# Kernel tuning notes

Hardware: AMD Instinct MI355X
Metric: run time of the kernel (lower is better)

## Reference

```python
import jax, jax.numpy as jnp
import numpy as np

NEG = -1e9


def _siglu(x):
    return x * jax.nn.sigmoid(x)


def setup_inputs() -> dict:
    key = jax.random.key(0)
    ks = jax.random.split(key, 10)
    B, S, M, D = 2, 2048, 64, 1024
    sc = 0.02
    return {
        "tokens": jax.random.normal(ks[0], (B, S, D), jnp.float32),
        "memory": jax.random.normal(ks[1], (B, M, D), jnp.float32),
        "Wq": jax.random.normal(ks[2], (D, D), jnp.float32) * sc,
        "bq": jnp.zeros((D,), jnp.float32),
        "Wk": jax.random.normal(ks[3], (D, D), jnp.float32) * sc,
        "bk": jnp.zeros((D,), jnp.float32),
        "Wv": jax.random.normal(ks[4], (D, D), jnp.float32) * sc,
        "bv": jnp.zeros((D,), jnp.float32),
        "Wo": jax.random.normal(ks[5], (D, D), jnp.float32) * sc,
        "bo": jnp.zeros((D,), jnp.float32),
        "pool_q": jax.random.normal(ks[6], (M, D), jnp.float32),
        "cell_W": jax.random.normal(ks[7], (2 * D, 2 * D), jnp.float32) * sc,
        "cell_b": jnp.zeros((2 * D,), jnp.float32),
    }


def reference(tokens, memory, Wq, bq, Wk, bk, Wv, bv, Wo, bo, pool_q, cell_W, cell_b):
    B, S, D = tokens.shape
    M = memory.shape[1]
    H = 16
    hd = D // H
    T = M + S

    x = jnp.concatenate([memory, tokens], axis=1)  # (B, T, D)

    # combined causal mask: memory rows/cols fully visible, token block causal
    tok_mask = jnp.triu(jnp.full((S, S), NEG, jnp.float32), k=1)
    mask = jnp.zeros((T, T), jnp.float32).at[M:, M:].set(tok_mask)  # (T, T)

    def heads(w, b):
        return (x @ w.T + b).reshape(B, T, H, hd).transpose(0, 2, 1, 3)

    q = heads(Wq, bq)  # (B, H, T, hd)
    k = heads(Wk, bk)
    v = heads(Wv, bv)

    scores = jnp.einsum("bhqd,bhkd->bhqk", q, k) * (hd ** -0.5) + mask
    attn = jax.nn.softmax(scores, axis=-1)
    ctx = jnp.einsum("bhqk,bhkd->bhqd", attn, v)
    ctx = ctx.transpose(0, 2, 1, 3).reshape(B, T, D)
    attn_out = ctx @ Wo.T + bo

    x = x + attn_out  # residual
    mem_out = x[:, :M]  # (B, M, D)
    tok_out = x[:, M:]  # (B, S, D)

    # attention pooling: one learnable query per memory slot
    pscores = jnp.einsum("md,bsd->bms", pool_q, tok_out) * (D ** -0.5)
    pweights = jax.nn.softmax(pscores, axis=-1)
    summary = jnp.einsum("bms,bsd->bmd", pweights, tok_out)  # (B, M, D)

    # MinimalRNNCell (siglu-gated) applied per memory slot
    combined = jnp.concatenate([mem_out, summary], axis=-1)  # (B, M, 2D)
    update = combined @ cell_W.T + cell_b
    gate, cand = jnp.split(update, 2, axis=-1)
    gate = jax.nn.sigmoid(gate)
    new_memory = mem_out * gate + (1.0 - gate) * _siglu(cand)

    return tok_out, new_memory
```

## Files before the change

kernel.cpp:

```cpp
#include <hip/hip_runtime.h>
#include <hip/hip_bf16.h>

#define B_  2
#define S_  2048
#define M_  64
#define D_  1024
#define T_  2112
#define H_  16
#define HD_ 64
#define BT_ (B_*T_)
#define NEGBIG (-1e9f)
#define LOG2E 1.44269504f

typedef float f32x4  __attribute__((ext_vector_type(4)));
typedef short short8 __attribute__((ext_vector_type(8)));
typedef unsigned short u16x4 __attribute__((ext_vector_type(4)));
typedef __bf16 bf16x8 __attribute__((ext_vector_type(8)));

typedef unsigned short TileBuf[2][128][64];

static __device__ __forceinline__ unsigned short bf16_of(float f) {
  __hip_bfloat16 h = __float2bfloat16(f);
  return __builtin_bit_cast(unsigned short, h);
}

static __device__ __forceinline__ f32x4 mfma_bf16(short8 a, short8 b, f32x4 c) {
  return __builtin_amdgcn_mfma_f32_16x16x32_bf16(
      __builtin_bit_cast(bf16x8, a), __builtin_bit_cast(bf16x8, b), c, 0, 0, 0);
}

static __device__ __forceinline__ void gload16(const void* g, void* lds) {
  __builtin_amdgcn_global_load_lds(
      (const __attribute__((address_space(1))) unsigned int*)g,
      (__attribute__((address_space(3))) unsigned int*)lds, 16, 0, 0);
}


__global__ void k_build_x(const float* __restrict__ tokens,
                          const float* __restrict__ memory,
                          unsigned short* __restrict__ xb) {
  for (int i = blockIdx.x * blockDim.x + threadIdx.x; i < BT_ * D_;
       i += gridDim.x * blockDim.x) {
    int b = i / (T_ * D_);
    int rem = i - b * (T_ * D_);
    int t = rem / D_;
    int d = rem - t * D_;
    float v = (t < M_) ? memory[((size_t)b * M_ + t) * D_ + d]
                       : tokens[((size_t)b * S_ + (t - M_)) * D_ + d];
    xb[i] = bf16_of(v);
  }
}

__global__ void k_cast_all(const float* __restrict__ Wq, const float* __restrict__ Wk,
                           const float* __restrict__ Wv, const float* __restrict__ Wo,
                           const float* __restrict__ cW, const float* __restrict__ pq,
                           unsigned short* __restrict__ Wqkvb, unsigned short* __restrict__ Wob,
                           unsigned short* __restrict__ cWb, unsigned short* __restrict__ pqb) {
  const int NW = D_ * D_;
  const int NC = 4 * D_ * D_;
  const int NP = M_ * D_;
  const int total = 4 * NW + NC + NP;
  for (int i = blockIdx.x * blockDim.x + threadIdx.x; i < total;
       i += gridDim.x * blockDim.x) {
    if (i < 3 * NW) {
      int which = i >> 20, j = i & (NW - 1);
      const float* s = (which == 0) ? Wq : (which == 1) ? Wk : Wv;
      Wqkvb[i] = bf16_of(s[j]);
    } else if (i < 4 * NW) {
      int j = i - 3 * NW;
      Wob[j] = bf16_of(Wo[j]);
    } else if (i < 4 * NW + NC) {
      int j = i - 4 * NW;
      cWb[j] = bf16_of(cW[j]);
    } else {
      int j = i - 4 * NW - NC;
      pqb[j] = bf16_of(pq[j] * 0.03125f * LOG2E);
    }
  }
}

__device__ __forceinline__ void gemm128_core(TileBuf& As, TileBuf& Bs,
                                             const unsigned short* __restrict__ A,
                                             const unsigned short* __restrict__ BT,
                                             int K, int m0, int n0,
                                             f32x4 acc[4][4]) {
  const int tid = threadIdx.x;
  const int w = tid >> 6, l = tid & 63;
  const int wr = w >> 1, wc = w & 1;
  const int lr = l & 15, lg = l >> 4;
  f32x4 z; z[0] = z[1] = z[2] = z[3] = 0.f;
#pragma unroll
  for (int i = 0; i < 4; i++)
#pragma unroll
    for (int j = 0; j < 4; j++) acc[i][j] = z;

  auto stage = [&](int buf, int k0) {
#pragma unroll
    for (int c = 0; c < 4; c++) {
      int rbase = c * 32 + w * 8;
      int rr = rbase + (l >> 3);
      int u = (l & 7) ^ (rr & 7);
      gload16(&A[(size_t)(m0 + rr) * K + k0 + u * 8], &As[buf][rbase][0]);
      gload16(&BT[(size_t)(n0 + rr) * K + k0 + u * 8], &Bs[buf][rbase][0]);
    }
  };

  stage(0, 0);
  int cur = 0;
  const int NK = K >> 6;
  for (int kt = 0; kt < NK; kt++) {
    if (kt + 1 < NK) {
      stage(cur ^ 1, (kt + 1) << 6);
      asm volatile("s_waitcnt vmcnt(8)" ::: "memory");
    } else {
      asm volatile("s_waitcnt vmcnt(0)" ::: "memory");
    }
    __builtin_amdgcn_s_barrier();

    short8 a[4][2], b[4][2];
#pragma unroll
    for (int i = 0; i < 4; i++) {
      int row = wr * 64 + i * 16 + lr;
      int sw = row & 7;
#pragma unroll
      for (int kk = 0; kk < 2; kk++)
        a[i][kk] = *(const short8*)&As[cur][row][(((kk << 2) | lg) ^ sw) * 8];
    }
#pragma unroll
    for (int j = 0; j < 4; j++) {
      int row = wc * 64 + j * 16 + lr;
      int sw = row & 7;
#pragma unroll
      for (int kk = 0; kk < 2; kk++)
        b[j][kk] = *(const short8*)&Bs[cur][row][(((kk << 2) | lg) ^ sw) * 8];
    }
    __builtin_amdgcn_s_setprio(1);
#pragma unroll
    for (int kk = 0; kk < 2; kk++)
#pragma unroll
      for (int i = 0; i < 4; i++)
#pragma unroll
        for (int j = 0; j < 4; j++)
          acc[i][j] = mfma_bf16(a[i][kk], b[j][kk], acc[i][j]);
    __builtin_amdgcn_s_setprio(0);

    __builtin_amdgcn_s_barrier();
    cur ^= 1;
  }
}

__device__ __forceinline__ void gemm_core(const unsigned short* __restrict__ A,
                                          const unsigned short* __restrict__ BT,
                                          int ldk, int Klen, int m0, int n0,
                                          f32x4 acc[4]) {
  __shared__ __align__(16) unsigned short As[64][40];
  __shared__ __align__(16) unsigned short Bs[64][40];
  const int tid = threadIdx.x;
  const int w = tid >> 6, l = tid & 63;
  const int sr = tid >> 2, sc = (tid & 3) * 8;
  f32x4 z; z[0] = z[1] = z[2] = z[3] = 0.f;
  acc[0] = acc[1] = acc[2] = acc[3] = z;
  for (int k0 = 0; k0 < Klen; k0 += 32) {
    __syncthreads();
    *(short8*)&As[sr][sc] = *(const short8*)&A[(size_t)(m0 + sr) * ldk + k0 + sc];
    *(short8*)&Bs[sr][sc] = *(const short8*)&BT[(size_t)(n0 + sr) * ldk + k0 + sc];
    __syncthreads();
    short8 a = *(const short8*)&As[w * 16 + (l & 15)][(l >> 4) * 8];
#pragma unroll
    for (int n = 0; n < 4; n++) {
      short8 b = *(const short8*)&Bs[n * 16 + (l & 15)][(l >> 4) * 8];
      acc[n] = mfma_bf16(a, b, acc[n]);
    }
  }
}

__global__ __launch_bounds__(256) void k_qk(
    const unsigned short* __restrict__ xb, const unsigned short* __restrict__ Wqkvb,
    const float* __restrict__ bq, const float* __restrict__ bk,
    unsigned short* __restrict__ qg, unsigned short* __restrict__ kg) {
  __shared__ __align__(16) TileBuf As;
  __shared__ __align__(16) TileBuf Bs;
  const int which = blockIdx.x >> 3;
  const unsigned short* W = Wqkvb + (size_t)which * D_ * D_;
  const float* bias = (which == 0) ? bq : bk;
  f32x4 acc[4][4];
  const int m0 = blockIdx.y * 128, n0 = (blockIdx.x & 7) * 128;
  gemm128_core(As, Bs, xb, W, D_, m0, n0, acc);
  const int tid = threadIdx.x, w = tid >> 6, l = tid & 63;
  const int wr = w >> 1, wc = w & 1;
#pragma unroll
  for (int i = 0; i < 4; i++) {
#pragma unroll
    for (int j = 0; j < 4; j++) {
#pragma unroll
      for (int r = 0; r < 4; r++) {
        int m = m0 + wr * 64 + i * 16 + (l >> 4) * 4 + r;
        int c = n0 + wc * 64 + j * 16 + (l & 15);
        int b = (m >= T_) ? 1 : 0;
        int t = m - b * T_;
        int h = c >> 6, dh = c & 63;
        int bh = b * H_ + h;
        float v = acc[i][j][r] + bias[c];
        if (which == 0)
          qg[((size_t)bh * T_ + t) * HD_ + dh] = bf16_of(v * 0.125f * LOG2E);
        else
          kg[((size_t)bh * T_ + t) * HD_ + dh] = bf16_of(v);
      }
    }
  }
}

__global__ __launch_bounds__(256) void k_v(
    const unsigned short* __restrict__ xb, const unsigned short* __restrict__ Wqkvb,
    const float* __restrict__ bv, unsigned short* __restrict__ vTg) {
  __shared__ __align__(16) TileBuf As;
  __shared__ __align__(16) TileBuf Bs;
  f32x4 acc[4][4];
  const int m0 = blockIdx.y * 128, n0 = blockIdx.x * 128;
  gemm128_core(As, Bs, xb, Wqkvb + (size_t)2 * D_ * D_, D_, m0, n0, acc);
  const int tid = threadIdx.x, w = tid >> 6, l = tid & 63;
  const int wr = w >> 1, wc = w & 1, lr = l & 15, lg = l >> 4;
  unsigned short* tr = &As[0][0][0];
#pragma unroll
  for (int i = 0; i < 4; i++) {
    int u = wr * 16 + i * 4 + lg;
#pragma unroll
    for (int j = 0; j < 4; j++) {
      int c = wc * 64 + j * 16 + lr;
      u16x4 pk;
#pragma unroll
      for (int r = 0; r < 4; r++) pk[r] = bf16_of(acc[i][j][r] + bv[n0 + c]);
      *(u16x4*)&tr[(size_t)c * 128 + (u ^ (c & 15)) * 4] = pk;
    }
  }
  __syncthreads();
  const int c = tid >> 1, hs = tid & 1;
  const int cg = n0 + c;
  const int h = cg >> 6, dh = cg & 63;
#pragma unroll
  for (int q = 0; q < 8; q++) {
    int ch = hs * 8 + q;
    int uu0 = (2 * ch) ^ (c & 15), uu1 = (2 * ch + 1) ^ (c & 15);
    u16x4 a0 = *(const u16x4*)&tr[(size_t)c * 128 + uu0 * 4];
    u16x4 a1 = *(const u16x4*)&tr[(size_t)c * 128 + uu1 * 4];
    short8 ov;
#pragma unroll
    for (int k = 0; k < 4; k++) { ov[k] = a0[k]; ov[4 + k] = a1[k]; }
    int mg = m0 + ch * 8;
    int b = (mg >= T_) ? 1 : 0;
    int t = mg - b * T_;
    *(short8*)&vTg[((size_t)(b * H_ + h) * HD_ + dh) * T_ + t] = ov;
  }
}

__global__ __launch_bounds__(256) void k_attn(
    const unsigned short* __restrict__ qg, const unsigned short* __restrict__ kg,
    const unsigned short* __restrict__ vTg, unsigned short* __restrict__ ctx) {
  const int id = blockIdx.x;
  const int xcd = id & 7;
  const int rem = id >> 3;
  const int g = rem / 33, qtr = rem - g * 33;
  const int qt = (qtr == 0) ? 0 : 33 - qtr;
  const int bh = g * 8 + xcd;
  const int tid = threadIdx.x, w = tid >> 6, l = tid & 63;
  const int lr = l & 15, lg = l >> 4;
  __shared__ __align__(16) unsigned short Ks[2][64][64];
  __shared__ __align__(16) unsigned short Vs[2][64][64];
  __shared__ __align__(16) unsigned short Ps[4][16][72];

  const unsigned short* qb = qg + (size_t)bh * T_ * HD_;
  const unsigned short* kb = kg + (size_t)bh * T_ * HD_;
  const unsigned short* vb = vTg + (size_t)bh * HD_ * T_;

  short8 aq[2];
  const int qrow = qt * 64 + w * 16 + lr;
#pragma unroll
  for (int st = 0; st < 2; st++)
    aq[st] = *(const short8*)&qb[(size_t)qrow * HD_ + st * 32 + lg * 8];

  f32x4 zz; zz[0] = zz[1] = zz[2] = zz[3] = 0.f;
  f32x4 o[4];
  o[0] = o[1] = o[2] = o[3] = zz;
  float mrun = -1e30f, lrun = 0.f;

  const int nkt = (qt == 0) ? 33 : qt + 1;

  auto stage = [&](int buf, int kb2) {
#pragma unroll
    for (int i = 0; i < 2; i++) {
      int rr = w * 16 + i * 8 + (l >> 3);
      int swz = ((l & 7) ^ (rr & 7)) * 8;
      gload16(&kb[(size_t)(kb2 + rr) * HD_ + swz], &Ks[buf][w * 16 + i * 8][0]);
      gload16(&vb[(size_t)rr * T_ + kb2 + swz], &Vs[buf][w * 16 + i * 8][0]);
    }
  };

  stage(0, 0);
  __syncthreads();
  int cur = 0;

  for (int j = 0; j < nkt; j++) {
    const int kbase = j * 64;
    if (j + 1 < nkt) stage(cur ^ 1, kbase + 64);

    short8 bkf[2][4];
#pragma unroll
    for (int n = 0; n < 4; n++) {
      int row = n * 16 + lr;
      int sw = lr & 7;
#pragma unroll
      for (int st = 0; st < 2; st++)
        bkf[st][n] = *(const short8*)&Ks[cur][row][((st * 4 + lg) ^ sw) * 8];
    }
    f32x4 s[4];
    s[0] = s[1] = s[2] = s[3] = zz;
    __builtin_amdgcn_s_setprio(1);
#pragma unroll
    for (int st = 0; st < 2; st++)
#pragma unroll
      for (int n = 0; n < 4; n++)
        s[n] = mfma_bf16(bkf[st][n], aq[st], s[n]);
    __builtin_amdgcn_s_setprio(0);

    if (qt > 0 && j == qt) {
      const int tql = w * 16 + lr;
#pragma unroll
      for (int n = 0; n < 4; n++)
#pragma unroll
        for (int r = 0; r < 4; r++) {
          int tkl = n * 16 + lg * 4 + r;
          if (tkl > tql) s[n][r] = NEGBIG;
        }
    }
    float pm = s[0][0];
#pragma unroll
    for (int n = 0; n < 4; n++)
#pragma unroll
      for (int r = 0; r < 4; r++) pm = fmaxf(pm, s[n][r]);
    pm = fmaxf(pm, __shfl_xor(pm, 16));
    pm = fmaxf(pm, __shfl_xor(pm, 32));

    if (__any(pm > mrun + 8.f)) {
      float mn = fmaxf(mrun, pm);
      float fac = exp2f(mrun - mn);
      mrun = mn;
      lrun *= fac;
      float fr[4];
#pragma unroll
      for (int r = 0; r < 4; r++) fr[r] = __shfl(fac, lg * 4 + r);
#pragma unroll
      for (int n = 0; n < 4; n++)
#pragma unroll
        for (int r = 0; r < 4; r++) o[n][r] *= fr[r];
    }
#pragma unroll
    for (int n = 0; n < 4; n++) {
      u16x4 pk;
#pragma unroll
      for (int r = 0; r < 4; r++) {
        float p = exp2f(s[n][r] - mrun);
        lrun += p;
        pk[r] = bf16_of(p);
      }
      *(u16x4*)&Ps[w][lr][n * 16 + lg * 4] = pk;
    }

    short8 bvf[2][4];
#pragma unroll
    for (int n = 0; n < 4; n++) {
      int row = n * 16 + lr;
      int sw = lr & 7;
#pragma unroll
      for (int st = 0; st < 2; st++)
        bvf[st][n] = *(const short8*)&Vs[cur][row][((st * 4 + lg) ^ sw) * 8];
    }
    short8 ap[2];
#pragma unroll
    for (int st = 0; st < 2; st++)
      ap[st] = *(const short8*)&Ps[w][lr][st * 32 + lg * 8];
    __builtin_amdgcn_s_setprio(1);
#pragma unroll
    for (int st = 0; st < 2; st++)
#pragma unroll
      for (int n = 0; n < 4; n++)
        o[n] = mfma_bf16(ap[st], bvf[st][n], o[n]);
    __builtin_amdgcn_s_setprio(0);

    __syncthreads();
    cur ^= 1;
  }
  lrun += __shfl_xor(lrun, 16);
  lrun += __shfl_xor(lrun, 32);
  float linv[4];
#pragma unroll
  for (int r = 0; r < 4; r++) linv[r] = 1.f / __shfl(lrun, lg * 4 + r);

  const int b = bh >> 4, h = bh & 15;
#pragma unroll
  for (int n = 0; n < 4; n++)
#pragma unroll
    for (int r = 0; r < 4; r++) {
      int tq = qt * 64 + w * 16 + lg * 4 + r;
      float val = o[n][r] * linv[r];
      ctx[((size_t)(b * T_ + tq)) * D_ + h * HD_ + n * 16 + lr] = bf16_of(val);
    }
}

__global__ __launch_bounds__(256) void k_out(
    const unsigned short* __restrict__ ctxb, const unsigned short* __restrict__ Wob,
    const float* __restrict__ bo, const float* __restrict__ tokens,
    const float* __restrict__ memory, float* __restrict__ out_tok,
    unsigned short* __restrict__ tokb, unsigned short* __restrict__ tokTb,
    float* __restrict__ memout, unsigned short* __restrict__ comb) {
  __shared__ __align__(16) TileBuf As;
  __shared__ __align__(16) TileBuf Bs;
  f32x4 acc[4][4];
  const int m0 = blockIdx.y * 128, n0 = blockIdx.x * 128;
  gemm128_core(As, Bs, ctxb, Wob, D_, m0, n0, acc);
  const int tid = threadIdx.x, w = tid >> 6, l = tid & 63;
  const int wr = w >> 1, wc = w & 1, lr = l & 15, lg = l >> 4;
  unsigned short* tr = &As[0][0][0];
#pragma unroll
  for (int i = 0; i < 4; i++) {
    int u = wr * 16 + i * 4 + lg;
#pragma unroll
    for (int j = 0; j < 4; j++) {
      int c = n0 + wc * 64 + j * 16 + lr;
      int cl = c - n0;
      u16x4 pk;
#pragma unroll
      for (int r = 0; r < 4; r++) {
        int m = m0 + wr * 64 + i * 16 + lg * 4 + r;
        int b = (m >= T_) ? 1 : 0;
        int t = m - b * T_;
        float xo = (t < M_) ? memory[((size_t)b * M_ + t) * D_ + c]
                            : tokens[((size_t)b * S_ + (t - M_)) * D_ + c];
        float val = acc[i][j][r] + bo[c] + xo;
        unsigned short vb16 = bf16_of(val);
        pk[r] = vb16;
        if (t < M_) {
          memout[((size_t)b * M_ + t) * D_ + c] = val;
          comb[((size_t)b * M_ + t) * (2 * D_) + c] = vb16;
        } else {
          size_t ti = (size_t)b * S_ + (t - M_);
          out_tok[ti * D_ + c] = val;
          tokb[ti * D_ + c] = vb16;
        }
      }
      *(u16x4*)&tr[(size_t)cl * 128 + (u ^ (cl & 15)) * 4] = pk;
    }
  }
  __syncthreads();
  const int cl = tid >> 1, hs = tid & 1;
  const int cg = n0 + cl;
#pragma unroll
  for (int q = 0; q < 8; q++) {
    int ch = hs * 8 + q;
    int mg = m0 + ch * 8;
    int b = (mg >= T_) ? 1 : 0;
    int t = mg - b * T_;
    if (t < M_) continue;
    int uu0 = (2 * ch) ^ (cl & 15), uu1 = (2 * ch + 1) ^ (cl & 15);
    u16x4 a0 = *(const u16x4*)&tr[(size_t)cl * 128 + uu0 * 4];
    u16x4 a1 = *(const u16x4*)&tr[(size_t)cl * 128 + uu1 * 4];
    short8 ov;
#pragma unroll
    for (int k = 0; k < 4; k++) { ov[k] = a0[k]; ov[4 + k] = a1[k]; }
    *(short8*)&tokTb[((size_t)b * D_ + cg) * S_ + (t - M_)] = ov;
  }
}

__global__ __launch_bounds__(256) void k_pscore_part(
    const unsigned short* __restrict__ pqb, const unsigned short* __restrict__ tokb,
    float* __restrict__ pscp) {
  const int stile = blockIdx.x, ks = blockIdx.y, b = blockIdx.z;
  f32x4 acc[4];
  gemm_core(pqb + ks * 256, tokb + (size_t)b * S_ * D_ + ks * 256, D_, 256,
            0, stile * 64, acc);
  const int tid = threadIdx.x, w = tid >> 6, l = tid & 63;
  float* dst = pscp + ((size_t)(ks * B_ + b) * M_) * S_;
#pragma unroll
  for (int n = 0; n < 4; n++) {
#pragma unroll
    for (int r = 0; r < 4; r++) {
      int m = w * 16 + (l >> 4) * 4 + r;
      int s = stile * 64 + n * 16 + (l & 15);
      dst[(size_t)m * S_ + s] = acc[n][r];
    }
  }
}

__global__ __launch_bounds__(256) void k_psoftmax(const float* __restrict__ pscp,
                                                  unsigned short* __restrict__ pw) {
  const int row = blockIdx.x;
  const int b = row >> 6, m = row & 63;
  const int tid = threadIdx.x;
  float v[8];
  float mx = -1e30f;
#pragma unroll
  for (int i = 0; i < 8; i++) {
    int s = tid + i * 256;
    float acc = 0.f;
#pragma unroll
    for (int ks = 0; ks < 4; ks++)
      acc += pscp[((size_t)(ks * B_ + b) * M_ + m) * S_ + s];
    v[i] = acc;
    mx = fmaxf(mx, acc);
  }
#pragma unroll
  for (int off = 1; off < 64; off <<= 1) mx = fmaxf(mx, __shfl_xor(mx, off));
  __shared__ float rm[4], rs[4];
  if ((tid & 63) == 0) rm[tid >> 6] = mx;
  __syncthreads();
  mx = fmaxf(fmaxf(rm[0], rm[1]), fmaxf(rm[2], rm[3]));
  float sum = 0.f;
#pragma unroll
  for (int i = 0; i < 8; i++) {
    v[i] = exp2f(v[i] - mx);
    sum += v[i];
  }
#pragma unroll
  for (int off = 1; off < 64; off <<= 1) sum += __shfl_xor(sum, off);
  if ((tid & 63) == 0) rs[tid >> 6] = sum;
  __syncthreads();
  float inv = 1.f / (rs[0] + rs[1] + rs[2] + rs[3]);
#pragma unroll
  for (int i = 0; i < 8; i++)
    pw[(size_t)row * S_ + tid + i * 256] = bf16_of(v[i] * inv);
}

__global__ __launch_bounds__(256) void k_summary_part(
    const unsigned short* __restrict__ pw, const unsigned short* __restrict__ tokTb,
    float* __restrict__ sump) {
  const int nt = blockIdx.x, ks = blockIdx.y, b = blockIdx.z;
  f32x4 acc[4];
  gemm_core(pw + (size_t)b * M_ * S_ + ks * 256,
            tokTb + (size_t)b * D_ * S_ + ks * 256, S_, 256, 0, nt * 64, acc);
  const int tid = threadIdx.x, w = tid >> 6, l = tid & 63;
  float* dst = sump + ((size_t)(ks * B_ + b) * M_) * D_;
#pragma unroll
  for (int n = 0; n < 4; n++) {
#pragma unroll
    for (int r = 0; r < 4; r++) {
      int m = w * 16 + (l >> 4) * 4 + r;
      int c = nt * 64 + n * 16 + (l & 15);
      dst[(size_t)m * D_ + c] = acc[n][r];
    }
  }
}

__global__ void k_sumcomb(const float* __restrict__ sump,
                          unsigned short* __restrict__ comb) {
  int i = blockIdx.x * blockDim.x + threadIdx.x;
  if (i >= B_ * M_ * D_) return;
  int bm = i >> 10, c = i & 1023;
  int b = bm >> 6, m = bm & 63;
  float acc = 0.f;
#pragma unroll
  for (int ks = 0; ks < 8; ks++)
    acc += sump[((size_t)(ks * B_ + b) * M_ + m) * D_ + c];
  comb[((size_t)b * M_ + m) * (2 * D_) + D_ + c] = bf16_of(acc);
}

__global__ __launch_bounds__(256) void k_cell_part(
    const unsigned short* __restrict__ comb, const unsigned short* __restrict__ cWb,
    float* __restrict__ cellp) {
  const int nt = blockIdx.x, mt = blockIdx.y, ks = blockIdx.z;
  f32x4 acc[4];
  gemm_core(comb + ks * 512, cWb + ks * 512, 2 * D_, 512, mt * 64, nt * 64, acc);
  const int tid = threadIdx.x, w = tid >> 6, l = tid & 63;
#pragma unroll
  for (int n = 0; n < 4; n++) {
#pragma unroll
    for (int r = 0; r < 4; r++) {
      int m = mt * 64 + w * 16 + (l >> 4) * 4 + r;
      int c = nt * 64 + n * 16 + (l & 15);
      cellp[((size_t)ks * (B_ * M_) + m) * (2 * D_) + c] = acc[n][r];
    }
  }
}

__global__ void k_newmem(const float* __restrict__ cellp,
                         const float* __restrict__ cb,
                         const float* __restrict__ memout,
                         float* __restrict__ out2) {
  int i = blockIdx.x * blockDim.x + threadIdx.x;
  if (i >= B_ * M_ * D_) return;
  int r = i >> 10, d = i & 1023;
  float gsum = cb[d], csum = cb[D_ + d];
#pragma unroll
  for (int ks = 0; ks < 4; ks++) {
    gsum += cellp[((size_t)ks * (B_ * M_) + r) * (2 * D_) + d];
    csum += cellp[((size_t)ks * (B_ * M_) + r) * (2 * D_) + D_ + d];
  }
  float sg = 1.f / (1.f + __expf(-gsum));
  float sc = 1.f / (1.f + __expf(-csum));
  out2[i] = memout[i] * sg + (1.f - sg) * (csum * sc);
}

extern "C" void kernel_launch(void* const* d_in, const int* in_sizes, int n_in,
                              void* d_out, int out_size, void* d_ws, size_t ws_size,
                              hipStream_t stream) {
  const float* tokens = (const float*)d_in[0];
  const float* memory = (const float*)d_in[1];
  const float* Wq = (const float*)d_in[2];
  const float* bq = (const float*)d_in[3];
  const float* Wk = (const float*)d_in[4];
  const float* bk = (const float*)d_in[5];
  const float* Wv = (const float*)d_in[6];
  const float* bv = (const float*)d_in[7];
  const float* Wo = (const float*)d_in[8];
  const float* bo = (const float*)d_in[9];
  const float* pool_q = (const float*)d_in[10];
  const float* cell_W = (const float*)d_in[11];
  const float* cell_b = (const float*)d_in[12];

  size_t off = 0;
  auto alloc = [&](size_t bytes) -> void* {
    void* p = (char*)d_ws + off;
    off += (bytes + 255) & ~(size_t)255;
    return p;
  };
  unsigned short* xb    = (unsigned short*)alloc((size_t)BT_ * D_ * 2);
  unsigned short* Wqkvb = (unsigned short*)alloc((size_t)3 * D_ * D_ * 2);
  unsigned short* Wob   = (unsigned short*)alloc((size_t)D_ * D_ * 2);
  unsigned short* cWb   = (unsigned short*)alloc((size_t)(2 * D_) * (2 * D_) * 2);
  unsigned short* pqb   = (unsigned short*)alloc((size_t)M_ * D_ * 2);
  unsigned short* qg    = (unsigned short*)alloc((size_t)B_ * H_ * T_ * HD_ * 2);
  unsigned short* kg    = (unsigned short*)alloc((size_t)B_ * H_ * T_ * HD_ * 2);
  unsigned short* vTg   = (unsigned short*)alloc((size_t)B_ * H_ * HD_ * T_ * 2);
  unsigned short* ctxb  = (unsigned short*)alloc((size_t)BT_ * D_ * 2);
  unsigned short* tokb  = (unsigned short*)alloc((size_t)B_ * S_ * D_ * 2);
  unsigned short* tokTb = (unsigned short*)alloc((size_t)B_ * D_ * S_ * 2);
  float*          memout= (float*)alloc((size_t)B_ * M_ * D_ * 4);
  unsigned short* comb  = (unsigned short*)alloc((size_t)B_ * M_ * 2 * D_ * 2);
  unsigned short* pwt   = (unsigned short*)alloc((size_t)B_ * M_ * S_ * 2);
  float*          pscp  = (float*)alloc((size_t)4 * B_ * M_ * S_ * 4);
  float*          sump  = (float*)alloc((size_t)8 * B_ * M_ * D_ * 4);
  float*          cellp = (float*)alloc((size_t)4 * B_ * M_ * 2 * D_ * 4);

  float* out_tok = (float*)d_out;
  float* out_mem = out_tok + (size_t)B_ * S_ * D_;

  k_build_x<<<2048, 256, 0, stream>>>(tokens, memory, xb);
  k_cast_all<<<4096, 256, 0, stream>>>(Wq, Wk, Wv, Wo, cell_W, pool_q,
                                       Wqkvb, Wob, cWb, pqb);

  k_qk<<<dim3(16, 33), 256, 0, stream>>>(xb, Wqkvb, bq, bk, qg, kg);
  k_v<<<dim3(8, 33), 256, 0, stream>>>(xb, Wqkvb, bv, vTg);
  k_attn<<<1056, 256, 0, stream>>>(qg, kg, vTg, ctxb);
  k_out<<<dim3(8, 33), 256, 0, stream>>>(ctxb, Wob, bo, tokens, memory, out_tok,
                                         tokb, tokTb, memout, comb);
  k_pscore_part<<<dim3(32, 4, 2), 256, 0, stream>>>(pqb, tokb, pscp);
  k_psoftmax<<<B_ * M_, 256, 0, stream>>>(pscp, pwt);
  k_summary_part<<<dim3(16, 8, 2), 256, 0, stream>>>(pwt, tokTb, sump);
  k_sumcomb<<<512, 256, 0, stream>>>(sump, comb);
  k_cell_part<<<dim3(32, 2, 4), 256, 0, stream>>>(comb, cWb, cellp);
  k_newmem<<<512, 256, 0, stream>>>(cellp, cell_b, memout, out_mem);
}
```

Before: 225.4 us.

## Enlarge attention query tile to 128 rows per block for K/V reuse

The attention kernel now processes 128 query rows per block, 32 per wave as two 16-row MFMA sub-tiles, instead of 64. Each staged K/V tile is reused by twice as many queries, which halves K/V global and LDS traffic per query and halves the block count. In exchange, register pressure rises and there are fewer blocks for load balance. The causal masking is generalised, the last tile is clamped and guarded because T is not a multiple of 128, and the P buffer in LDS gets an XOR swizzle.

```diff
diff --git a/kernel.cpp b/kernel.cpp
--- a/kernel.cpp
+++ b/kernel.cpp
@@ -259,31 +259,39 @@
   const int id = blockIdx.x;
   const int xcd = id & 7;
   const int rem = id >> 3;
-  const int g = rem / 33, qtr = rem - g * 33;
-  const int qt = (qtr == 0) ? 0 : 33 - qtr;
+  const int g = rem / 17, qir = rem - g * 17;
+  const int qt = (qir == 0) ? 0 : 17 - qir;
   const int bh = g * 8 + xcd;
   const int tid = threadIdx.x, w = tid >> 6, l = tid & 63;
   const int lr = l & 15, lg = l >> 4;
   __shared__ __align__(16) unsigned short Ks[2][64][64];
   __shared__ __align__(16) unsigned short Vs[2][64][64];
-  __shared__ __align__(16) unsigned short Ps[4][16][72];
+  __shared__ __align__(16) unsigned short Ps[4][32][64];
 
   const unsigned short* qb = qg + (size_t)bh * T_ * HD_;
   const unsigned short* kb = kg + (size_t)bh * T_ * HD_;
   const unsigned short* vb = vTg + (size_t)bh * HD_ * T_;
 
-  short8 aq[2];
-  const int qrow = qt * 64 + w * 16 + lr;
-#pragma unroll
-  for (int st = 0; st < 2; st++)
-    aq[st] = *(const short8*)&qb[(size_t)qrow * HD_ + st * 32 + lg * 8];
+  short8 aq[2][2];
+#pragma unroll
+  for (int mi = 0; mi < 2; mi++) {
+    int tq = qt * 128 + w * 32 + mi * 16 + lr;
+    int tqc = (tq < T_) ? tq : T_ - 1;
+#pragma unroll
+    for (int st = 0; st < 2; st++)
+      aq[mi][st] = *(const short8*)&qb[(size_t)tqc * HD_ + st * 32 + lg * 8];
+  }
 
   f32x4 zz; zz[0] = zz[1] = zz[2] = zz[3] = 0.f;
-  f32x4 o[4];
-  o[0] = o[1] = o[2] = o[3] = zz;
-  float mrun = -1e30f, lrun = 0.f;
-
-  const int nkt = (qt == 0) ? 33 : qt + 1;
+  f32x4 o[2][4];
+#pragma unroll
+  for (int mi = 0; mi < 2; mi++)
+#pragma unroll
+    for (int n = 0; n < 4; n++) o[mi][n] = zz;
+  float mrun[2] = {-1e30f, -1e30f}, lrun[2] = {0.f, 0.f};
+
+  const int nkt = (qt == 0) ? 33 : ((2 * qt + 2 < 33) ? 2 * qt + 2 : 33);
+  const int qmin = (qt == 0) ? M_ : qt * 128;
 
   auto stage = [&](int buf, int kb2) {
 #pragma unroll
@@ -312,57 +320,78 @@
       for (int st = 0; st < 2; st++)
         bkf[st][n] = *(const short8*)&Ks[cur][row][((st * 4 + lg) ^ sw) * 8];
     }
-    f32x4 s[4];
-    s[0] = s[1] = s[2] = s[3] = zz;
+    f32x4 s[2][4];
+#pragma unroll
+    for (int mi = 0; mi < 2; mi++)
+#pragma unroll
+      for (int n = 0; n < 4; n++) s[mi][n] = zz;
     __builtin_amdgcn_s_setprio(1);
 #pragma unroll
     for (int st = 0; st < 2; st++)
 #pragma unroll
+      for (int mi = 0; mi < 2; mi++)
+#pragma unroll
+        for (int n = 0; n < 4; n++)
+          s[mi][n] = mfma_bf16(bkf[st][n], aq[mi][st], s[mi][n]);
+    __builtin_amdgcn_s_setprio(0);
+
+    if (kbase + 63 > qmin) {
+#pragma unroll
+      for (int mi = 0; mi < 2; mi++) {
+        const int tq = qt * 128 + w * 32 + mi * 16 + lr;
+#pragma unroll
+        for (int n = 0; n < 4; n++)
+#pragma unroll
+          for (int r = 0; r < 4; r++) {
+            int tk = kbase + n * 16 + lg * 4 + r;
+            if (tq >= M_ && tk > tq) s[mi][n][r] = NEGBIG;
+          }
+      }
+    }
+    float pm[2];
+#pragma unroll
+    for (int mi = 0; mi < 2; mi++) {
+      float p = s[mi][0][0];
+#pragma unroll
       for (int n = 0; n < 4; n++)
-        s[n] = mfma_bf16(bkf[st][n], aq[st], s[n]);
-    __builtin_amdgcn_s_setprio(0);
-
-    if (qt > 0 && j == qt) {
-      const int tql = w * 16 + lr;
-#pragma unroll
-      for (int n = 0; n < 4; n++)
+#pragma unroll
+        for (int r = 0; r < 4; r++) p = fmaxf(p, s[mi][n][r]);
+      p = fmaxf(p, __shfl_xor(p, 16));
+      p = fmaxf(p, __shfl_xor(p, 32));
+      pm[mi] = p;
+    }
+    bool need = (pm[0] > mrun[0] + 8.f) || (pm[1] > mrun[1] + 8.f);
+    if (__any(need)) {
+#pragma unroll
+      for (int mi = 0; mi < 2; mi++) {
+        float mn = fmaxf(mrun[mi], pm[mi]);
+        float fac = exp2f(mrun[mi] - mn);
+        mrun[mi] = mn;
+        lrun[mi] *= fac;
+        float fr[4];
+#pragma unroll
+        for (int r = 0; r < 4; r++) fr[r] = __shfl(fac, lg * 4 + r);
+#pragma unroll
+        for (int n = 0; n < 4; n++)
+#pragma unroll
+          for (int r = 0; r < 4; r++) o[mi][n][r] *= fr[r];
+      }
+    }
+#pragma unroll
+    for (int mi = 0; mi < 2; mi++) {
+      const int row = mi * 16 + lr;
+      const int hsw = (row & 7) ^ ((row >> 3) & 3);
+#pragma unroll
+      for (int n = 0; n < 4; n++) {
+        u16x4 pk;
 #pragma unroll
         for (int r = 0; r < 4; r++) {
-          int tkl = n * 16 + lg * 4 + r;
-          if (tkl > tql) s[n][r] = NEGBIG;
+          float p = exp2f(s[mi][n][r] - mrun[mi]);
+          lrun[mi] += p;
+          pk[r] = bf16_of(p);
         }
-    }
-    float pm = s[0][0];
-#pragma unroll
-    for (int n = 0; n < 4; n++)
-#pragma unroll
-      for (int r = 0; r < 4; r++) pm = fmaxf(pm, s[n][r]);
-    pm = fmaxf(pm, __shfl_xor(pm, 16));
-    pm = fmaxf(pm, __shfl_xor(pm, 32));
-
-    if (__any(pm > mrun + 8.f)) {
-      float mn = fmaxf(mrun, pm);
-      float fac = exp2f(mrun - mn);
-      mrun = mn;
-      lrun *= fac;
-      float fr[4];
-#pragma unroll
-      for (int r = 0; r < 4; r++) fr[r] = __shfl(fac, lg * 4 + r);
-#pragma unroll
-      for (int n = 0; n < 4; n++)
-#pragma unroll
-        for (int r = 0; r < 4; r++) o[n][r] *= fr[r];
-    }
-#pragma unroll
-    for (int n = 0; n < 4; n++) {
-      u16x4 pk;
-#pragma unroll
-      for (int r = 0; r < 4; r++) {
-        float p = exp2f(s[n][r] - mrun);
-        lrun += p;
-        pk[r] = bf16_of(p);
+        *(u16x4*)&Ps[w][row][((n * 4 + lg) ^ (2 * hsw)) * 4] = pk;
       }
-      *(u16x4*)&Ps[w][lr][n * 16 + lg * 4] = pk;
     }
 
     short8 bvf[2][4];
@@ -374,36 +403,49 @@
       for (int st = 0; st < 2; st++)
         bvf[st][n] = *(const short8*)&Vs[cur][row][((st * 4 + lg) ^ sw) * 8];
     }
-    short8 ap[2];
+    short8 ap[2][2];
+#pragma unroll
+    for (int mi = 0; mi < 2; mi++) {
+      const int row = mi * 16 + lr;
+      const int hsw = (row & 7) ^ ((row >> 3) & 3);
+#pragma unroll
+      for (int st = 0; st < 2; st++) {
+        int ub = (st * 8 + lg * 2) ^ (2 * hsw);
+        ap[mi][st] = *(const short8*)&Ps[w][row][ub * 4];
+      }
+    }
+    __builtin_amdgcn_s_setprio(1);
 #pragma unroll
     for (int st = 0; st < 2; st++)
-      ap[st] = *(const short8*)&Ps[w][lr][st * 32 + lg * 8];
-    __builtin_amdgcn_s_setprio(1);
-#pragma unroll
-    for (int st = 0; st < 2; st++)
-#pragma unroll
-      for (int n = 0; n < 4; n++)
-        o[n] = mfma_bf16(ap[st], bvf[st][n], o[n]);
+#pragma unroll
+      for (int mi = 0; mi < 2; mi++)
+#pragma unroll
+        for (int n = 0; n < 4; n++)
+          o[mi][n] = mfma_bf16(ap[mi][st], bvf[st][n], o[mi][n]);
     __builtin_amdgcn_s_setprio(0);
 
     __syncthreads();
     cur ^= 1;
   }
-  lrun += __shfl_xor(lrun, 16);
-  lrun += __shfl_xor(lrun, 32);
-  float linv[4];
-#pragma unroll
-  for (int r = 0; r < 4; r++) linv[r] = 1.f / __shfl(lrun, lg * 4 + r);
-
   const int b = bh >> 4, h = bh & 15;
 #pragma unroll
-  for (int n = 0; n < 4; n++)
-#pragma unroll
-    for (int r = 0; r < 4; r++) {
-      int tq = qt * 64 + w * 16 + lg * 4 + r;
-      float val = o[n][r] * linv[r];
-      ctx[((size_t)(b * T_ + tq)) * D_ + h * HD_ + n * 16 + lr] = bf16_of(val);
-    }
+  for (int mi = 0; mi < 2; mi++) {
+    lrun[mi] += __shfl_xor(lrun[mi], 16);
+    lrun[mi] += __shfl_xor(lrun[mi], 32);
+    float linv[4];
+#pragma unroll
+    for (int r = 0; r < 4; r++) linv[r] = 1.f / __shfl(lrun[mi], lg * 4 + r);
+#pragma unroll
+    for (int n = 0; n < 4; n++)
+#pragma unroll
+      for (int r = 0; r < 4; r++) {
+        int tq = qt * 128 + w * 32 + mi * 16 + lg * 4 + r;
+        if (tq < T_) {
+          float val = o[mi][n][r] * linv[r];
+          ctx[((size_t)(b * T_ + tq)) * D_ + h * HD_ + n * 16 + lr] = bf16_of(val);
+        }
+      }
+  }
 }
 
 __global__ __launch_bounds__(256) void k_out(
@@ -648,7 +690,7 @@
 
   k_qk<<<dim3(16, 33), 256, 0, stream>>>(xb, Wqkvb, bq, bk, qg, kg);
   k_v<<<dim3(8, 33), 256, 0, stream>>>(xb, Wqkvb, bv, vTg);
-  k_attn<<<1056, 256, 0, stream>>>(qg, kg, vTg, ctxb);
+  k_attn<<<544, 256, 0, stream>>>(qg, kg, vTg, ctxb);
   k_out<<<dim3(8, 33), 256, 0, stream>>>(ctxb, Wob, bo, tokens, memory, out_tok,
                                          tokb, tokTb, memout, comb);
   k_pscore_part<<<dim3(32, 4, 2), 256, 0, stream>>>(pqb, tokb, pscp);
```

New measurement: 250.8 us. 11.2% more time.
